# Performance work log

Measured on AMD Instinct MI355X. Metric: run time of the kernel, lower is better.

## Reference

```python
import jax, jax.numpy as jnp
import numpy as np

D_MODEL = 2048
D_HEAD = 128
NUM_HEADS = 16
D_LATENT = 512
B, S = 4, 2048


def setup_inputs() -> dict:
    key = jax.random.key(0)
    ks = jax.random.split(key, 11)
    sc = lambda fan_in: 1.0 / np.sqrt(fan_in)
    x = jax.random.normal(ks[0], (B, S, D_MODEL), dtype=jnp.float32)
    # weights stored as [in, out] (transpose of torch nn.Linear.weight)
    W_down = jax.random.uniform(ks[1], (D_MODEL, D_LATENT), jnp.float32, -sc(D_MODEL), sc(D_MODEL))
    b_down = jax.random.uniform(ks[2], (D_LATENT,), jnp.float32, -sc(D_MODEL), sc(D_MODEL))
    W_uk = jax.random.uniform(ks[3], (D_LATENT, D_MODEL), jnp.float32, -sc(D_LATENT), sc(D_LATENT))
    b_uk = jax.random.uniform(ks[4], (D_MODEL,), jnp.float32, -sc(D_LATENT), sc(D_LATENT))
    W_uv = jax.random.uniform(ks[5], (D_LATENT, D_MODEL), jnp.float32, -sc(D_LATENT), sc(D_LATENT))
    b_uv = jax.random.uniform(ks[6], (D_MODEL,), jnp.float32, -sc(D_LATENT), sc(D_LATENT))
    W_q = jax.random.uniform(ks[7], (D_MODEL, NUM_HEADS * D_HEAD), jnp.float32, -sc(D_MODEL), sc(D_MODEL))
    b_q = jax.random.uniform(ks[8], (NUM_HEADS * D_HEAD,), jnp.float32, -sc(D_MODEL), sc(D_MODEL))
    W_o = jax.random.uniform(ks[9], (NUM_HEADS * D_HEAD, D_MODEL), jnp.float32, -sc(NUM_HEADS * D_HEAD), sc(NUM_HEADS * D_HEAD))
    b_o = jax.random.uniform(ks[10], (D_MODEL,), jnp.float32, -sc(NUM_HEADS * D_HEAD), sc(NUM_HEADS * D_HEAD))
    return {"x": x, "W_down": W_down, "b_down": b_down, "W_uk": W_uk, "b_uk": b_uk,
            "W_uv": W_uv, "b_uv": b_uv, "W_q": W_q, "b_q": b_q, "W_o": W_o, "b_o": b_o}


def reference(x, W_down, b_down, W_uk, b_uk, W_uv, b_uv, W_q, b_q, W_o, b_o):
    b, s, _ = x.shape
    latents = x @ W_down + b_down                      # [B,S,L]
    keys = latents @ W_uk + b_uk                       # [B,S,D]
    values = latents @ W_uv + b_uv                     # [B,S,D]
    q = (x @ W_q + b_q).reshape(b, s, NUM_HEADS, D_HEAD).transpose(0, 2, 1, 3)
    k = keys.reshape(b, s, NUM_HEADS, D_HEAD).transpose(0, 2, 1, 3)
    v = values.reshape(b, s, NUM_HEADS, D_HEAD).transpose(0, 2, 1, 3)
    scores = jnp.einsum('bhqd,bhkd->bhqk', q, k) / np.sqrt(D_HEAD).astype(np.float32)
    attn = jax.nn.softmax(scores, axis=-1)
    ctx = jnp.einsum('bhqk,bhkd->bhqd', attn, v)       # [B,H,S,Dh]
    ctx = ctx.transpose(0, 2, 1, 3).reshape(b, s, NUM_HEADS * D_HEAD)
    return ctx @ W_o + b_o
```

## Files before the change

### kernel.cpp

```cpp
#include <hip/hip_runtime.h>

#define D_MODEL 2048
#define D_LATENT 512
#define NUM_HEADS 16
#define D_HEAD 128
#define BATCH 4
#define SEQ 2048
#define MTOK (BATCH*SEQ)

typedef __bf16 bf16_t;
typedef __bf16 bf16x4 __attribute__((ext_vector_type(4)));
typedef __bf16 bf16x8 __attribute__((ext_vector_type(8)));
typedef float  f32x4  __attribute__((ext_vector_type(4)));

__device__ __forceinline__ void load_lds16(const bf16_t* g, bf16_t* l) {
  __builtin_amdgcn_global_load_lds(
      (const __attribute__((address_space(1))) void*)g,
      (__attribute__((address_space(3))) void*)l,
      16, 0, 0);
}

__global__ void convert_f32_bf16_kernel(const float* __restrict__ src,
                                        bf16_t* __restrict__ dst, int n4) {
  int i = blockIdx.x * 256 + threadIdx.x;
  if (i >= n4) return;
  float4 v = *(const float4*)&src[(size_t)i * 4];
  bf16x4 o = { (bf16_t)v.x, (bf16_t)v.y, (bf16_t)v.z, (bf16_t)v.w };
  *(bf16x4*)&dst[(size_t)i * 4] = o;
}

__global__ void transpose_w_kernel(const float* __restrict__ src, bf16_t* __restrict__ dst,
                                   int R, int C) {
  __shared__ __align__(16) bf16_t tile[64][66];
  int rt = blockIdx.y * 64, ct = blockIdx.x * 64;
  int lc = threadIdx.x & 63, lr = threadIdx.x >> 6;
  for (int i = 0; i < 64; i += 4)
    tile[lr + i][lc] = (bf16_t)src[(size_t)(rt + lr + i) * C + ct + lc];
  __syncthreads();
  for (int i = 0; i < 64; i += 4)
    dst[(size_t)(ct + lr + i) * R + rt + lc] = tile[lc][lr + i];
}

__global__ void transpose_v_kernel(const bf16_t* __restrict__ v, bf16_t* __restrict__ vt) {
  __shared__ __align__(16) bf16_t tile[64][66];
  int bh = blockIdx.z; int b = bh >> 4, h = bh & 15;
  int st = blockIdx.x * 64, dt = blockIdx.y * 64;
  int lc = threadIdx.x & 63, lr = threadIdx.x >> 6;
  const bf16_t* src = v + (size_t)b * SEQ * D_MODEL + h * D_HEAD;
  for (int i = 0; i < 64; i += 4)
    tile[lr + i][lc] = src[(size_t)(st + lr + i) * D_MODEL + dt + lc];
  __syncthreads();
  bf16_t* dst = vt + (size_t)bh * D_HEAD * SEQ;
  for (int i = 0; i < 64; i += 4)
    dst[(size_t)(dt + lr + i) * SEQ + st + lc] = tile[lc][lr + i];
}

template<typename OutT>
__global__ __launch_bounds__(256, 2) void gemm_bt_kernel(
    const bf16_t* __restrict__ A, const bf16_t* __restrict__ Wt,
    const float* __restrict__ bias, OutT* __restrict__ C,
    int M, int N, int K, float premul)
{
  __shared__ __align__(16) bf16_t As[128 * 32];
  __shared__ __align__(16) bf16_t Bs[128 * 32];
  int tid = threadIdx.x;
  int lane = tid & 63, wave = tid >> 6;
  int wr = (wave >> 1) * 64, wc = (wave & 1) * 64;
  size_t row0 = (size_t)blockIdx.x * 128, col0 = (size_t)blockIdx.y * 128;
  int lr = lane & 15, quad = lane >> 4, rq = quad * 4;

  f32x4 acc[4][4] = {};

  int srow = wave * 32 + (lane >> 2);
  int scol = ((lane & 3) ^ ((lane >> 3) & 3)) * 8;
  const bf16_t* Ag = A  + (row0 + srow) * K + scol;
  const bf16_t* Bg = Wt + (col0 + srow) * K + scol;
  bf16_t* Asw = As + wave * 1024;
  bf16_t* Bsw = Bs + wave * 1024;

  int rchunk = (quad ^ ((lr >> 1) & 3)) * 8;

  for (int k0 = 0; k0 < K; k0 += 32) {
    __syncthreads();
    load_lds16(Ag,          Asw);
    load_lds16(Ag + 16 * K, Asw + 512);
    load_lds16(Bg,          Bsw);
    load_lds16(Bg + 16 * K, Bsw + 512);
    Ag += 32; Bg += 32;
    __syncthreads();

    bf16x8 af[4], bfr[4];
    #pragma unroll
    for (int mi = 0; mi < 4; ++mi)
      af[mi] = *(const bf16x8*)&As[(wr + mi * 16 + lr) * 32 + rchunk];
    #pragma unroll
    for (int ni = 0; ni < 4; ++ni)
      bfr[ni] = *(const bf16x8*)&Bs[(wc + ni * 16 + lr) * 32 + rchunk];
    #pragma unroll
    for (int mi = 0; mi < 4; ++mi)
      #pragma unroll
      for (int ni = 0; ni < 4; ++ni)
        acc[mi][ni] = __builtin_amdgcn_mfma_f32_16x16x32_bf16(af[mi], bfr[ni], acc[mi][ni], 0, 0, 0);
  }

  #pragma unroll
  for (int ni = 0; ni < 4; ++ni) {
    int col = (int)col0 + wc + ni * 16 + lr;
    float bv = bias[col];
    #pragma unroll
    for (int mi = 0; mi < 4; ++mi) {
      #pragma unroll
      for (int r = 0; r < 4; ++r) {
        size_t row = row0 + wr + mi * 16 + rq + r;
        C[row * N + col] = (OutT)((acc[mi][ni][r] + bv) * premul);
      }
    }
  }
}

__global__ __launch_bounds__(256, 2) void attention_kernel(
    const bf16_t* __restrict__ q, const bf16_t* __restrict__ keys,
    const bf16_t* __restrict__ vt, bf16_t* __restrict__ ctx)
{
  __shared__ __align__(16) bf16_t KS[2][64 * 128];
  __shared__ __align__(16) bf16_t VS[2][128 * 64];
  __shared__ __align__(16) bf16_t PS[128 * 64];
  int wg = blockIdx.x;
  int qt = (wg >> 3) & 15;
  int bh = (wg & 7) | ((wg >> 7) << 3);
  int b = bh >> 4, h = bh & 15;
  int tid = threadIdx.x, lane = tid & 63, wave = tid >> 6;
  int lr = lane & 15, quad = lane >> 4, kq = quad * 8, rq = quad * 4;
  int l7 = lr & 7;

  const bf16_t* qg = q    + (size_t)(b * SEQ + qt * 128) * D_MODEL + h * D_HEAD;
  const bf16_t* kg = keys + (size_t)b * SEQ * D_MODEL + h * D_HEAD;
  const bf16_t* vg = vt   + (size_t)bh * D_HEAD * SEQ;

  bf16x8 qf[2][4];
  #pragma unroll
  for (int mi = 0; mi < 2; ++mi)
    #pragma unroll
    for (int ks = 0; ks < 4; ++ks)
      qf[mi][ks] = *(const bf16x8*)&qg[(size_t)(wave*32 + mi*16 + lr) * D_MODEL + ks*32 + kq];

  bf16x8 kreg[4], vreg[4];
  const bf16_t* kp4[4];
  const bf16_t* vp4[4];
  int kdo[4], vdo[4];
  #pragma unroll
  for (int i = 0; i < 4; ++i) {
    int c = tid + i * 256;
    int r = c >> 4, kc = c & 15;
    kp4[i] = kg + (size_t)r * D_MODEL + kc * 8;
    kdo[i] = r * 128 + ((kc ^ (r & 7)) * 8);
    int d = c >> 3, vc = c & 7;
    vp4[i] = vg + (size_t)d * SEQ + vc * 8;
    vdo[i] = d * 64 + ((vc ^ (d & 7)) * 8);
  }

  #pragma unroll
  for (int i = 0; i < 4; ++i) {
    kreg[i] = *(const bf16x8*)kp4[i];
    vreg[i] = *(const bf16x8*)vp4[i];
  }
  #pragma unroll
  for (int i = 0; i < 4; ++i) {
    *(bf16x8*)&KS[0][kdo[i]] = kreg[i];
    *(bf16x8*)&VS[0][vdo[i]] = vreg[i];
  }
  #pragma unroll
  for (int i = 0; i < 4; ++i) {
    kp4[i] += 64 * D_MODEL;
    vp4[i] += 64;
    kreg[i] = *(const bf16x8*)kp4[i];
    vreg[i] = *(const bf16x8*)vp4[i];
  }

  f32x4 accO[2][8] = {};
  float m2[2]   = {-1e30f, -1e30f};
  float lsum[2] = {0.f, 0.f};

  __syncthreads();

  for (int kt = 0; kt < SEQ/64; ++kt) {
    const bf16_t* Kc = KS[kt & 1];
    const bf16_t* Vc = VS[kt & 1];
    bf16_t* Kn = KS[(kt & 1) ^ 1];
    bf16_t* Vn = VS[(kt & 1) ^ 1];

    f32x4 sc[2][4] = {};
    #pragma unroll
    for (int ks = 0; ks < 4; ++ks) {
      bf16x8 kf[4];
      #pragma unroll
      for (int ni = 0; ni < 4; ++ni)
        kf[ni] = *(const bf16x8*)&Kc[(ni*16 + lr) * 128 + (((ks*4 + quad) ^ l7) * 8)];
      __builtin_amdgcn_s_setprio(1);
      #pragma unroll
      for (int mi = 0; mi < 2; ++mi)
        #pragma unroll
        for (int ni = 0; ni < 4; ++ni)
          sc[mi][ni] = __builtin_amdgcn_mfma_f32_16x16x32_bf16(kf[ni], qf[mi][ks], sc[mi][ni], 0, 0, 0);
      __builtin_amdgcn_s_setprio(0);
    }

    if (kt + 1 < SEQ/64) {
      #pragma unroll
      for (int i = 0; i < 4; ++i) {
        *(bf16x8*)&Kn[kdo[i]] = kreg[i];
        *(bf16x8*)&VS[(kt & 1) ^ 1][vdo[i]] = vreg[i];
      }
    }
    (void)Vn;
    if (kt + 2 < SEQ/64) {
      #pragma unroll
      for (int i = 0; i < 4; ++i) {
        kp4[i] += 64 * D_MODEL;
        vp4[i] += 64;
        kreg[i] = *(const bf16x8*)kp4[i];
        vreg[i] = *(const bf16x8*)vp4[i];
      }
    }

    #pragma unroll
    for (int mi = 0; mi < 2; ++mi) {
      float rm = sc[mi][0][0];
      #pragma unroll
      for (int ni = 0; ni < 4; ++ni)
        #pragma unroll
        for (int r = 0; r < 4; ++r) rm = fmaxf(rm, sc[mi][ni][r]);
      rm = fmaxf(rm, __shfl_xor(rm, 16, 64));
      rm = fmaxf(rm, __shfl_xor(rm, 32, 64));

      if (!__all(rm - m2[mi] <= 8.0f)) {
        float mnew  = fmaxf(m2[mi], rm);
        float alpha = exp2f(m2[mi] - mnew);
        m2[mi] = mnew;
        lsum[mi] *= alpha;
        float ar[4];
        #pragma unroll
        for (int r = 0; r < 4; ++r) ar[r] = __shfl(alpha, rq + r, 16);
        #pragma unroll
        for (int nd = 0; nd < 8; ++nd)
          #pragma unroll
          for (int r = 0; r < 4; ++r) accO[mi][nd][r] *= ar[r];
      }

      float rs = 0.f;
      int prow = wave*32 + mi*16 + lr;
      int pbase = prow * 64;
      int psw = prow & 7;
      #pragma unroll
      for (int ni = 0; ni < 4; ++ni) {
        float p0 = exp2f(sc[mi][ni][0] - m2[mi]);
        float p1 = exp2f(sc[mi][ni][1] - m2[mi]);
        float p2 = exp2f(sc[mi][ni][2] - m2[mi]);
        float p3 = exp2f(sc[mi][ni][3] - m2[mi]);
        rs += (p0 + p1) + (p2 + p3);
        bf16x4 pk = { (bf16_t)p0, (bf16_t)p1, (bf16_t)p2, (bf16_t)p3 };
        *(bf16x4*)&PS[pbase + (((ni*2 + (quad>>1)) ^ psw) * 8) + (quad&1)*4] = pk;
      }
      rs += __shfl_xor(rs, 16, 64);
      rs += __shfl_xor(rs, 32, 64);
      lsum[mi] += rs;
    }

    #pragma unroll
    for (int ks2 = 0; ks2 < 2; ++ks2) {
      bf16x8 pf[2], vf[8];
      #pragma unroll
      for (int mi = 0; mi < 2; ++mi)
        pf[mi] = *(const bf16x8*)&PS[(wave*32 + mi*16 + lr) * 64 + (((ks2*4 + quad) ^ l7) * 8)];
      #pragma unroll
      for (int nd = 0; nd < 8; ++nd)
        vf[nd] = *(const bf16x8*)&Vc[(nd*16 + lr) * 64 + (((ks2*4 + quad) ^ l7) * 8)];
      __builtin_amdgcn_s_setprio(1);
      #pragma unroll
      for (int mi = 0; mi < 2; ++mi)
        #pragma unroll
        for (int nd = 0; nd < 8; ++nd)
          accO[mi][nd] = __builtin_amdgcn_mfma_f32_16x16x32_bf16(pf[mi], vf[nd], accO[mi][nd], 0, 0, 0);
      __builtin_amdgcn_s_setprio(0);
    }

    __syncthreads();
  }

  bf16_t* og = ctx + (size_t)(b * SEQ + qt * 128) * D_MODEL + h * D_HEAD;
  #pragma unroll
  for (int mi = 0; mi < 2; ++mi) {
    float inv[4];
    #pragma unroll
    for (int r = 0; r < 4; ++r) inv[r] = 1.0f / __shfl(lsum[mi], rq + r, 16);
    #pragma unroll
    for (int r = 0; r < 4; ++r) {
      int row = wave*32 + mi*16 + rq + r;
      #pragma unroll
      for (int nd = 0; nd < 8; ++nd)
        og[(size_t)row * D_MODEL + nd*16 + lr] = (bf16_t)(accO[mi][nd][r] * inv[r]);
    }
  }
}

extern "C" void kernel_launch(void* const* d_in, const int* in_sizes, int n_in,
                              void* d_out, int out_size, void* d_ws, size_t ws_size,
                              hipStream_t stream) {
  const float* x      = (const float*)d_in[0];
  const float* W_down = (const float*)d_in[1];
  const float* b_down = (const float*)d_in[2];
  const float* W_uk   = (const float*)d_in[3];
  const float* b_uk   = (const float*)d_in[4];
  const float* W_uv   = (const float*)d_in[5];
  const float* b_uv   = (const float*)d_in[6];
  const float* W_q    = (const float*)d_in[7];
  const float* b_q    = (const float*)d_in[8];
  const float* W_o    = (const float*)d_in[9];
  const float* b_o    = (const float*)d_in[10];
  float* out = (float*)d_out;

  char* ws = (char*)d_ws;
  bf16_t* xb      = (bf16_t*)ws;  ws += (size_t)MTOK*D_MODEL*2;
  bf16_t* Wt_down = (bf16_t*)ws;  ws += (size_t)D_LATENT*D_MODEL*2;
  bf16_t* Wt_uk   = (bf16_t*)ws;  ws += (size_t)D_MODEL*D_LATENT*2;
  bf16_t* Wt_uv   = (bf16_t*)ws;  ws += (size_t)D_MODEL*D_LATENT*2;
  bf16_t* Wt_q    = (bf16_t*)ws;  ws += (size_t)D_MODEL*D_MODEL*2;
  bf16_t* Wt_o    = (bf16_t*)ws;  ws += (size_t)D_MODEL*D_MODEL*2;
  bf16_t* lat     = (bf16_t*)ws;  ws += (size_t)MTOK*D_LATENT*2;
  bf16_t* keys    = (bf16_t*)ws;  ws += (size_t)MTOK*D_MODEL*2;
  bf16_t* vals    = (bf16_t*)ws;  ws += (size_t)MTOK*D_MODEL*2;
  bf16_t* qm      = (bf16_t*)ws;  ws += (size_t)MTOK*D_MODEL*2;
  bf16_t* vtm     = (bf16_t*)ws;  ws += (size_t)MTOK*D_MODEL*2;
  bf16_t* ctx     = vals;

  const float cs = 0.0883883476483184f * 1.44269504089f;

  convert_f32_bf16_kernel<<<(MTOK*D_MODEL/4 + 255)/256, 256, 0, stream>>>(x, xb, MTOK*D_MODEL/4);

  transpose_w_kernel<<<dim3(D_LATENT/64, D_MODEL/64), 256, 0, stream>>>(W_down, Wt_down, D_MODEL, D_LATENT);
  transpose_w_kernel<<<dim3(D_MODEL/64, D_LATENT/64), 256, 0, stream>>>(W_uk,   Wt_uk,   D_LATENT, D_MODEL);
  transpose_w_kernel<<<dim3(D_MODEL/64, D_LATENT/64), 256, 0, stream>>>(W_uv,   Wt_uv,   D_LATENT, D_MODEL);
  transpose_w_kernel<<<dim3(D_MODEL/64, D_MODEL/64),  256, 0, stream>>>(W_q,    Wt_q,    D_MODEL,  D_MODEL);
  transpose_w_kernel<<<dim3(D_MODEL/64, D_MODEL/64),  256, 0, stream>>>(W_o,    Wt_o,    D_MODEL,  D_MODEL);

  gemm_bt_kernel<bf16_t><<<dim3(MTOK/128, D_LATENT/128), 256, 0, stream>>>(xb,  Wt_down, b_down, lat,  MTOK, D_LATENT, D_MODEL, 1.0f);
  gemm_bt_kernel<bf16_t><<<dim3(MTOK/128, D_MODEL/128),  256, 0, stream>>>(lat, Wt_uk,   b_uk,   keys, MTOK, D_MODEL,  D_LATENT, 1.0f);
  gemm_bt_kernel<bf16_t><<<dim3(MTOK/128, D_MODEL/128),  256, 0, stream>>>(lat, Wt_uv,   b_uv,   vals, MTOK, D_MODEL,  D_LATENT, 1.0f);
  gemm_bt_kernel<bf16_t><<<dim3(MTOK/128, D_MODEL/128),  256, 0, stream>>>(xb,  Wt_q,    b_q,    qm,   MTOK, D_MODEL,  D_MODEL, cs);

  transpose_v_kernel<<<dim3(SEQ/64, D_HEAD/64, BATCH*NUM_HEADS), 256, 0, stream>>>(vals, vtm);

  attention_kernel<<<1024, 256, 0, stream>>>(qm, keys, vtm, ctx);

  gemm_bt_kernel<float><<<dim3(MTOK/128, D_MODEL/128), 256, 0, stream>>>(ctx, Wt_o, b_o, out, MTOK, D_MODEL, D_MODEL, 1.0f);
}
```

Before: 601.3 us.

## Batch weight transposes, fuse down/Q and K/V GEMMs, write V transposed directly

After: 560.9 us. 1.07x faster.

```diff
diff --git a/kernel.cpp b/kernel.cpp
--- a/kernel.cpp
+++ b/kernel.cpp
@@ -29,9 +29,23 @@
   *(bf16x4*)&dst[(size_t)i * 4] = o;
 }
 
-__global__ void transpose_w_kernel(const float* __restrict__ src, bf16_t* __restrict__ dst,
-                                   int R, int C) {
+__global__ void transpose_w_all(const float* __restrict__ a0, const float* __restrict__ a1,
+                                const float* __restrict__ a2, const float* __restrict__ a3,
+                                const float* __restrict__ a4,
+                                bf16_t* __restrict__ o0, bf16_t* __restrict__ o1,
+                                bf16_t* __restrict__ o2, bf16_t* __restrict__ o3,
+                                bf16_t* __restrict__ o4) {
   __shared__ __align__(16) bf16_t tile[64][66];
+  int z = blockIdx.z;
+  const float* src; bf16_t* dst; int R, C;
+  switch (z) {
+    case 0: src = a0; dst = o0; R = D_MODEL; C = D_LATENT; break;
+    case 1: src = a1; dst = o1; R = D_LATENT; C = D_MODEL; break;
+    case 2: src = a2; dst = o2; R = D_LATENT; C = D_MODEL; break;
+    case 3: src = a3; dst = o3; R = D_MODEL; C = D_MODEL; break;
+    default: src = a4; dst = o4; R = D_MODEL; C = D_MODEL; break;
+  }
+  if ((int)blockIdx.x * 64 >= C || (int)blockIdx.y * 64 >= R) return;
   int rt = blockIdx.y * 64, ct = blockIdx.x * 64;
   int lc = threadIdx.x & 63, lr = threadIdx.x >> 6;
   for (int i = 0; i < 64; i += 4)
@@ -41,19 +55,6 @@
     dst[(size_t)(ct + lr + i) * R + rt + lc] = tile[lc][lr + i];
 }
 
-__global__ void transpose_v_kernel(const bf16_t* __restrict__ v, bf16_t* __restrict__ vt) {
-  __shared__ __align__(16) bf16_t tile[64][66];
-  int bh = blockIdx.z; int b = bh >> 4, h = bh & 15;
-  int st = blockIdx.x * 64, dt = blockIdx.y * 64;
-  int lc = threadIdx.x & 63, lr = threadIdx.x >> 6;
-  const bf16_t* src = v + (size_t)b * SEQ * D_MODEL + h * D_HEAD;
-  for (int i = 0; i < 64; i += 4)
-    tile[lr + i][lc] = src[(size_t)(st + lr + i) * D_MODEL + dt + lc];
-  __syncthreads();
-  bf16_t* dst = vt + (size_t)bh * D_HEAD * SEQ;
-  for (int i = 0; i < 64; i += 4)
-    dst[(size_t)(dt + lr + i) * SEQ + st + lc] = tile[lc][lr + i];
-}
 
 template<typename OutT>
 __global__ __launch_bounds__(256, 2) void gemm_bt_kernel(
@@ -113,6 +114,178 @@
       for (int r = 0; r < 4; ++r) {
         size_t row = row0 + wr + mi * 16 + rq + r;
         C[row * N + col] = (OutT)((acc[mi][ni][r] + bv) * premul);
+      }
+    }
+  }
+}
+
+__global__ __launch_bounds__(256, 2) void gemm_dq_kernel(
+    const bf16_t* __restrict__ A, const bf16_t* __restrict__ WtD,
+    const bf16_t* __restrict__ WtQ, const float* __restrict__ biasD,
+    const float* __restrict__ biasQ, bf16_t* __restrict__ CD,
+    bf16_t* __restrict__ CQ, int M, float premulQ)
+{
+  const int K = D_MODEL;
+  __shared__ __align__(16) bf16_t As[128 * 32];
+  __shared__ __align__(16) bf16_t Bs[128 * 32];
+  int tid = threadIdx.x;
+  int lane = tid & 63, wave = tid >> 6;
+  int wr = (wave >> 1) * 64, wc = (wave & 1) * 64;
+  int yb = blockIdx.y;
+  bool isq = yb >= 4;
+  const bf16_t* Wt = isq ? WtQ : WtD;
+  const float* bias = isq ? biasQ : biasD;
+  bf16_t* C = isq ? CQ : CD;
+  int N = isq ? D_MODEL : D_LATENT;
+  float premul = isq ? premulQ : 1.0f;
+  size_t row0 = (size_t)blockIdx.x * 128, col0 = (size_t)(isq ? yb - 4 : yb) * 128;
+  int lr = lane & 15, quad = lane >> 4, rq = quad * 4;
+
+  f32x4 acc[4][4] = {};
+
+  int srow = wave * 32 + (lane >> 2);
+  int scol = ((lane & 3) ^ ((lane >> 3) & 3)) * 8;
+  const bf16_t* Ag = A  + (row0 + srow) * K + scol;
+  const bf16_t* Bg = Wt + (col0 + srow) * K + scol;
+  bf16_t* Asw = As + wave * 1024;
+  bf16_t* Bsw = Bs + wave * 1024;
+
+  int rchunk = (quad ^ ((lr >> 1) & 3)) * 8;
+
+  for (int k0 = 0; k0 < K; k0 += 32) {
+    __syncthreads();
+    load_lds16(Ag,          Asw);
+    load_lds16(Ag + 16 * K, Asw + 512);
+    load_lds16(Bg,          Bsw);
+    load_lds16(Bg + 16 * K, Bsw + 512);
+    Ag += 32; Bg += 32;
+    __syncthreads();
+
+    bf16x8 af[4], bfr[4];
+    #pragma unroll
+    for (int mi = 0; mi < 4; ++mi)
+      af[mi] = *(const bf16x8*)&As[(wr + mi * 16 + lr) * 32 + rchunk];
+    #pragma unroll
+    for (int ni = 0; ni < 4; ++ni)
+      bfr[ni] = *(const bf16x8*)&Bs[(wc + ni * 16 + lr) * 32 + rchunk];
+    #pragma unroll
+    for (int mi = 0; mi < 4; ++mi)
+      #pragma unroll
+      for (int ni = 0; ni < 4; ++ni)
+        acc[mi][ni] = __builtin_amdgcn_mfma_f32_16x16x32_bf16(af[mi], bfr[ni], acc[mi][ni], 0, 0, 0);
+  }
+
+  #pragma unroll
+  for (int ni = 0; ni < 4; ++ni) {
+    int col = (int)col0 + wc + ni * 16 + lr;
+    float bv = bias[col];
+    #pragma unroll
+    for (int mi = 0; mi < 4; ++mi) {
+      #pragma unroll
+      for (int r = 0; r < 4; ++r) {
+        size_t row = row0 + wr + mi * 16 + rq + r;
+        C[row * N + col] = (bf16_t)((acc[mi][ni][r] + bv) * premul);
+      }
+    }
+  }
+}
+
+__global__ __launch_bounds__(256, 2) void gemm_kv_kernel(
+    const bf16_t* __restrict__ A, const bf16_t* __restrict__ WtK,
+    const bf16_t* __restrict__ WtV, const float* __restrict__ biasK,
+    const float* __restrict__ biasV, bf16_t* __restrict__ keysO,
+    bf16_t* __restrict__ vtO, int M)
+{
+  const int K = D_LATENT;
+  __shared__ __align__(16) bf16_t As[128 * 32];
+  __shared__ __align__(16) bf16_t Bs[128 * 32];
+  __shared__ __align__(16) bf16_t E[64 * 136];
+  int tid = threadIdx.x;
+  int lane = tid & 63, wave = tid >> 6;
+  int wr = (wave >> 1) * 64, wc = (wave & 1) * 64;
+  int yb = blockIdx.y;
+  bool isv = yb >= 16;
+  const bf16_t* Wt = isv ? WtV : WtK;
+  const float* bias = isv ? biasV : biasK;
+  size_t row0 = (size_t)blockIdx.x * 128, col0 = (size_t)(isv ? yb - 16 : yb) * 128;
+  int lr = lane & 15, quad = lane >> 4, rq = quad * 4;
+
+  f32x4 acc[4][4] = {};
+
+  int srow = wave * 32 + (lane >> 2);
+  int scol = ((lane & 3) ^ ((lane >> 3) & 3)) * 8;
+  const bf16_t* Ag = A  + (row0 + srow) * K + scol;
+  const bf16_t* Bg = Wt + (col0 + srow) * K + scol;
+  bf16_t* Asw = As + wave * 1024;
+  bf16_t* Bsw = Bs + wave * 1024;
+
+  int rchunk = (quad ^ ((lr >> 1) & 3)) * 8;
+
+  for (int k0 = 0; k0 < K; k0 += 32) {
+    __syncthreads();
+    load_lds16(Ag,          Asw);
+    load_lds16(Ag + 16 * K, Asw + 512);
+    load_lds16(Bg,          Bsw);
+    load_lds16(Bg + 16 * K, Bsw + 512);
+    Ag += 32; Bg += 32;
+    __syncthreads();
+
+    bf16x8 af[4], bfr[4];
+    #pragma unroll
+    for (int mi = 0; mi < 4; ++mi)
+      af[mi] = *(const bf16x8*)&As[(wr + mi * 16 + lr) * 32 + rchunk];
+    #pragma unroll
+    for (int ni = 0; ni < 4; ++ni)
+      bfr[ni] = *(const bf16x8*)&Bs[(wc + ni * 16 + lr) * 32 + rchunk];
+    #pragma unroll
+    for (int mi = 0; mi < 4; ++mi)
+      #pragma unroll
+      for (int ni = 0; ni < 4; ++ni)
+        acc[mi][ni] = __builtin_amdgcn_mfma_f32_16x16x32_bf16(af[mi], bfr[ni], acc[mi][ni], 0, 0, 0);
+  }
+
+  if (!isv) {
+    #pragma unroll
+    for (int ni = 0; ni < 4; ++ni) {
+      int col = (int)col0 + wc + ni * 16 + lr;
+      float bv = bias[col];
+      #pragma unroll
+      for (int mi = 0; mi < 4; ++mi) {
+        #pragma unroll
+        for (int r = 0; r < 4; ++r) {
+          size_t row = row0 + wr + mi * 16 + rq + r;
+          keysO[row * D_MODEL + col] = (bf16_t)(acc[mi][ni][r] + bv);
+        }
+      }
+    }
+  } else {
+    int b = (int)(row0 >> 11);
+    int s0 = (int)(row0 & 2047);
+    int h = yb - 16;
+    bf16_t* vtb = vtO + (size_t)(b * NUM_HEADS + h) * D_HEAD * SEQ;
+    #pragma unroll
+    for (int h2 = 0; h2 < 2; ++h2) {
+      __syncthreads();
+      if ((wave & 1) == h2) {
+        #pragma unroll
+        for (int ni = 0; ni < 4; ++ni) {
+          int dh = ni * 16 + lr;
+          float bv = bias[(int)col0 + h2 * 64 + dh];
+          #pragma unroll
+          for (int mi = 0; mi < 4; ++mi) {
+            #pragma unroll
+            for (int r = 0; r < 4; ++r) {
+              int s = wr + mi * 16 + rq + r;
+              E[dh * 136 + s] = (bf16_t)(acc[mi][ni][r] + bv);
+            }
+          }
+        }
+      }
+      __syncthreads();
+      for (int t = tid; t < 1024; t += 256) {
+        int d = t >> 4, ch = t & 15;
+        bf16x8 v = *(const bf16x8*)&E[d * 136 + ch * 8];
+        *(bf16x8*)&vtb[(size_t)(h2 * 64 + d) * SEQ + s0 + ch * 8] = v;
       }
     }
   }
@@ -187,7 +360,6 @@
     const bf16_t* Kc = KS[kt & 1];
     const bf16_t* Vc = VS[kt & 1];
     bf16_t* Kn = KS[(kt & 1) ^ 1];
-    bf16_t* Vn = VS[(kt & 1) ^ 1];
 
     f32x4 sc[2][4] = {};
     #pragma unroll
@@ -212,7 +384,6 @@
         *(bf16x8*)&VS[(kt & 1) ^ 1][vdo[i]] = vreg[i];
       }
     }
-    (void)Vn;
     if (kt + 2 < SEQ/64) {
       #pragma unroll
       for (int i = 0; i < 4; ++i) {
@@ -337,18 +508,14 @@
 
   convert_f32_bf16_kernel<<<(MTOK*D_MODEL/4 + 255)/256, 256, 0, stream>>>(x, xb, MTOK*D_MODEL/4);
 
-  transpose_w_kernel<<<dim3(D_LATENT/64, D_MODEL/64), 256, 0, stream>>>(W_down, Wt_down, D_MODEL, D_LATENT);
-  transpose_w_kernel<<<dim3(D_MODEL/64, D_LATENT/64), 256, 0, stream>>>(W_uk,   Wt_uk,   D_LATENT, D_MODEL);
-  transpose_w_kernel<<<dim3(D_MODEL/64, D_LATENT/64), 256, 0, stream>>>(W_uv,   Wt_uv,   D_LATENT, D_MODEL);
-  transpose_w_kernel<<<dim3(D_MODEL/64, D_MODEL/64),  256, 0, stream>>>(W_q,    Wt_q,    D_MODEL,  D_MODEL);
-  transpose_w_kernel<<<dim3(D_MODEL/64, D_MODEL/64),  256, 0, stream>>>(W_o,    Wt_o,    D_MODEL,  D_MODEL);
-
-  gemm_bt_kernel<bf16_t><<<dim3(MTOK/128, D_LATENT/128), 256, 0, stream>>>(xb,  Wt_down, b_down, lat,  MTOK, D_LATENT, D_MODEL, 1.0f);
-  gemm_bt_kernel<bf16_t><<<dim3(MTOK/128, D_MODEL/128),  256, 0, stream>>>(lat, Wt_uk,   b_uk,   keys, MTOK, D_MODEL,  D_LATENT, 1.0f);
-  gemm_bt_kernel<bf16_t><<<dim3(MTOK/128, D_MODEL/128),  256, 0, stream>>>(lat, Wt_uv,   b_uv,   vals, MTOK, D_MODEL,  D_LATENT, 1.0f);
-  gemm_bt_kernel<bf16_t><<<dim3(MTOK/128, D_MODEL/128),  256, 0, stream>>>(xb,  Wt_q,    b_q,    qm,   MTOK, D_MODEL,  D_MODEL, cs);
-
-  transpose_v_kernel<<<dim3(SEQ/64, D_HEAD/64, BATCH*NUM_HEADS), 256, 0, stream>>>(vals, vtm);
+  transpose_w_all<<<dim3(32, 32, 5), 256, 0, stream>>>(
+      W_down, W_uk, W_uv, W_q, W_o, Wt_down, Wt_uk, Wt_uv, Wt_q, Wt_o);
+
+  gemm_dq_kernel<<<dim3(MTOK/128, 4 + D_MODEL/128), 256, 0, stream>>>(
+      xb, Wt_down, Wt_q, b_down, b_q, lat, qm, MTOK, cs);
+
+  gemm_kv_kernel<<<dim3(MTOK/128, 32), 256, 0, stream>>>(
+      lat, Wt_uk, Wt_uv, b_uk, b_uv, keys, vtm, MTOK);
 
   attention_kernel<<<1024, 256, 0, stream>>>(qm, keys, vtm, ctx);
 
```
